# Optimization experiments

Hardware: AMD Instinct MI355X
Metric: run time of the kernel (lower is better)

Reference implementation:

```python
import jax, jax.numpy as jnp
import numpy as np

EPS = 1e-5


def conv2d(x, w, b, groups=1):
    # x: NCHW, w: OIHW, stride 1, SAME padding (== padding=k//2 for odd k)
    y = jax.lax.conv_general_dilated(
        x, w, window_strides=(1, 1), padding='SAME',
        dimension_numbers=('NCHW', 'OIHW', 'NCHW'),
        feature_group_count=groups)
    return y + b[None, :, None, None]


def gelu(x):
    return jax.nn.gelu(x, approximate=False)  # torch default GELU is exact erf


def adaptive_feature_norm(x, gamma, beta, s1w, s1b, s2w, s2b):
    # stats_net: GAP -> 1x1 conv -> ReLU -> 1x1 conv -> chunk into (gamma_a, beta_a)
    pooled = x.mean(axis=(2, 3), keepdims=True)                 # [B,C,1,1]
    h = jax.nn.relu(conv2d(pooled, s1w, s1b))
    stats = conv2d(h, s2w, s2b)                                 # [B,2C,1,1]
    ag, ab = jnp.split(stats, 2, axis=1)
    mean = x.mean(axis=(2, 3), keepdims=True)
    n = x.shape[2] * x.shape[3]
    var = ((x - mean) ** 2).sum(axis=(2, 3), keepdims=True) / (n - 1)  # unbiased, torch.var_mean default
    x_norm = (x - mean) * jax.lax.rsqrt(var + EPS)
    return (1 + ag) * gamma * x_norm + ab * beta


def setup_inputs() -> dict:
    key = jax.random.key(0)
    ks = jax.random.split(key, 40)
    B, C, H, W = 16, 256, 96, 96
    c4 = C // 4

    def n(k, shape, s=0.02):
        return jax.random.normal(k, shape, dtype=jnp.float32) * s

    inp = dict(
        x=jax.random.normal(ks[0], (B, C, H, W), dtype=jnp.float32),
        # branch1 conv1: dim -> dim//4, 3x3
        b1_conv1_w=n(ks[1], (c4, C, 3, 3)), b1_conv1_b=jnp.zeros((c4,), jnp.float32),
        # AFN on dim//4
        afn1_gamma=jnp.ones((1, c4, 1, 1), jnp.float32), afn1_beta=jnp.zeros((1, c4, 1, 1), jnp.float32),
        afn1_s1_w=n(ks[2], (c4 // 4, c4, 1, 1)), afn1_s1_b=jnp.zeros((c4 // 4,), jnp.float32),
        afn1_s2_w=n(ks[3], (c4 * 2, c4 // 4, 1, 1)), afn1_s2_b=jnp.zeros((c4 * 2,), jnp.float32),
        # branch1 conv2: dim//4 -> dim, 3x3
        b1_conv2_w=n(ks[4], (C, c4, 3, 3)), b1_conv2_b=jnp.zeros((C,), jnp.float32),
        # AFN on dim
        afn2_gamma=jnp.ones((1, C, 1, 1), jnp.float32), afn2_beta=jnp.zeros((1, C, 1, 1), jnp.float32),
        afn2_s1_w=n(ks[5], (c4, C, 1, 1)), afn2_s1_b=jnp.zeros((c4,), jnp.float32),
        afn2_s2_w=n(ks[6], (C * 2, c4, 1, 1)), afn2_s2_b=jnp.zeros((C * 2,), jnp.float32),
        # attention qkv/proj (1x1 convs)
        qkv_w=n(ks[7], (3 * C, C, 1, 1)), qkv_b=jnp.zeros((3 * C,), jnp.float32),
        proj_w=n(ks[8], (C, C, 1, 1)), proj_b=jnp.zeros((C,), jnp.float32),
        # 3 frequency decomposition branches, stacked
        # grouped 3x3 conv: groups=C//4, in=C (4 per group), out=C//4 (1 per group) -> weight [C//4, 4, 3, 3]
        fd_dw_w=n(ks[9], (3, c4, 4, 3, 3)), fd_dw_b=jnp.zeros((3, c4), jnp.float32),
        fd_pw_w=n(ks[10], (3, C, c4, 1, 1)), fd_pw_b=jnp.zeros((3, C), jnp.float32),
        freq_weights=jnp.ones((3,), jnp.float32),
        # router: GAP -> 1x1 conv -> softmax over 2 routes
        router_w=n(ks[11], (2, C, 1, 1)), router_b=jnp.zeros((2,), jnp.float32),
    )
    return inp


def reference(x,
              b1_conv1_w, b1_conv1_b, afn1_gamma, afn1_beta, afn1_s1_w, afn1_s1_b, afn1_s2_w, afn1_s2_b,
              b1_conv2_w, b1_conv2_b, afn2_gamma, afn2_beta, afn2_s1_w, afn2_s1_b, afn2_s2_w, afn2_s2_b,
              qkv_w, qkv_b, proj_w, proj_b, fd_dw_w, fd_dw_b, fd_pw_w, fd_pw_b, freq_weights,
              router_w, router_b):
    B, C, H, W = x.shape
    num_heads = 8
    hd = C // num_heads
    scale = C ** (-0.5)

    # ---- router ----
    pooled = x.mean(axis=(2, 3), keepdims=True)
    route = jax.nn.softmax(conv2d(pooled, router_w, router_b), axis=1)  # [B,2,1,1]

    # ---- branch1: conv -> AFN -> GELU -> conv -> AFN ----
    h = conv2d(x, b1_conv1_w, b1_conv1_b)
    h = adaptive_feature_norm(h, afn1_gamma, afn1_beta, afn1_s1_w, afn1_s1_b, afn1_s2_w, afn1_s2_b)
    h = gelu(h)
    h = conv2d(h, b1_conv2_w, b1_conv2_b)
    out1 = adaptive_feature_norm(h, afn2_gamma, afn2_beta, afn2_s1_w, afn2_s1_b, afn2_s2_w, afn2_s2_b)

    # ---- branch2: multi-scale frequency attention ----
    qkv = conv2d(x, qkv_w, qkv_b).reshape(B, 3, num_heads, hd, H, W)
    q, k, v = qkv[:, 0], qkv[:, 1], qkv[:, 2]          # [B, nh, hd, H, W]
    # attn over spatial rows: q @ k^T contracts W -> [B, nh, hd, H, H]
    attn = jnp.einsum('bndhw,bndgw->bndhg', q, k) * scale
    attn = jax.nn.softmax(attn, axis=-1)
    a = jnp.einsum('bndhg,bndgw->bndhw', attn, v)       # [B, nh, hd, H, W]
    # torch: .transpose(1, 2).reshape(B, C, H, W)  (hd-major channel order)
    a = a.transpose(0, 2, 1, 3, 4).reshape(B, C, H, W)
    x_attn = conv2d(a, proj_w, proj_b)

    fw = jax.nn.softmax(freq_weights, axis=0)
    freq_out = 0.0
    for i in range(3):
        f = conv2d(x, fd_dw_w[i], fd_dw_b[i], groups=C // 4)
        f = conv2d(gelu(f), fd_pw_w[i], fd_pw_b[i])
        freq_out = freq_out + fw[i] * f
    out2 = x_attn + freq_out

    return x + route[:, 0:1, :, :] * out1 + route[:, 1:2, :, :] * out2
```

## Files before the change

### kernel.cpp

```cpp
#include <hip/hip_runtime.h>
#include <hip/hip_bf16.h>
#include <math.h>
#include <stdint.h>

#define BB 16
#define CC 256
#define C4 64
#define HH 96
#define WW 96
#define HW 9216
#define EPSF 1e-5f

using bf16x8 = __attribute__((ext_vector_type(8))) short;
using bf16x4 = __attribute__((ext_vector_type(4))) short;
using f32x4  = __attribute__((ext_vector_type(4))) float;

#define GLD16(g, l) \
    __builtin_amdgcn_global_load_lds((const __attribute__((address_space(1))) unsigned int*)(g), \
                                     (__attribute__((address_space(3))) unsigned int*)(l), 16, 0, 0)

__device__ inline float bf2f_bits(short s) {
    return __uint_as_float(((unsigned int)(unsigned short)s) << 16);
}
__device__ inline short f2bf_bits(float f) {
    unsigned int u = __float_as_uint(f);
    return (short)((u + 0x7fffu + ((u >> 16) & 1u)) >> 16);
}

__global__ void zero_n_kernel(unsigned int* __restrict__ p, int n) {
    int i = blockIdx.x * 256 + threadIdx.x;
    if (i < n) p[i] = 0u;
}

__global__ void router_kernel(const float* __restrict__ pooled, const float* __restrict__ rw,
                              const float* __restrict__ rb, const float* __restrict__ fwts,
                              float* __restrict__ route, float* __restrict__ fw) {
    int t = threadIdx.x;
    const float invhw = 1.f / (float)HW;
    if (t < BB) {
        float l0 = rb[0], l1 = rb[1];
        for (int c = 0; c < CC; ++c) {
            float p = pooled[t * CC + c] * invhw;
            l0 += p * rw[c];
            l1 += p * rw[CC + c];
        }
        float m = fmaxf(l0, l1);
        float e0 = __expf(l0 - m), e1 = __expf(l1 - m);
        float inv = 1.f / (e0 + e1);
        route[t * 2 + 0] = e0 * inv;
        route[t * 2 + 1] = e1 * inv;
    }
    if (t == BB) {
        float a = fwts[0], b = fwts[1], c = fwts[2];
        float m = fmaxf(a, fmaxf(b, c));
        float e0 = __expf(a - m), e1 = __expf(b - m), e2 = __expf(c - m);
        float inv = 1.f / (e0 + e1 + e2);
        fw[0] = e0 * inv; fw[1] = e1 * inv; fw[2] = e2 * inv;
    }
}

__global__ void pack_w3x3_kernel(const float* __restrict__ w, __hip_bfloat16* __restrict__ wt,
                                 int COUT, int CINW) {
    int idx = blockIdx.x * 256 + threadIdx.x;
    int total = COUT * 9 * CINW;
    if (idx >= total) return;
    int ci = idx % CINW; int rest = idx / CINW; int tau = rest % 9; int co = rest / 9;
    wt[idx] = __float2bfloat16(w[((size_t)co * CINW + ci) * 9 + tau]);
}

__global__ void cast_w_kernel(const float* __restrict__ w, __hip_bfloat16* __restrict__ o, int n) {
    int idx = blockIdx.x * 256 + threadIdx.x;
    if (idx < n) o[idx] = __float2bfloat16(w[idx]);
}

__global__ void cast_w448_kernel(const float* __restrict__ w, __hip_bfloat16* __restrict__ A448) {
    int idx = blockIdx.x * 256 + threadIdx.x;
    int co = idx >> 8, ci = idx & 255;
    A448[co * 448 + ci] = __float2bfloat16(w[idx]);
}

__global__ void fuse_freq_w448_kernel(const float* __restrict__ pww, const float* __restrict__ pwb,
                                      const float* __restrict__ pjb, const float* __restrict__ fw,
                                      __hip_bfloat16* __restrict__ A448, float* __restrict__ fb448) {
    int co = blockIdx.x; int t = threadIdx.x;
    int i = t >> 6, g = t & 63;
    A448[co * 448 + 256 + t] = __float2bfloat16(fw[i] * pww[((size_t)(i * 256 + co)) * 64 + g]);
    if (t == 0) fb448[co] = pjb[co] + fw[0] * pwb[co] + fw[1] * pwb[256 + co] + fw[2] * pwb[512 + co];
}

__device__ inline float to_f32(float v) { return v; }
__device__ inline float to_f32(__hip_bfloat16 v) { return __bfloat162float(v); }

template <typename TIN, int CIN, int OSTR, bool POOL, bool AFN, bool GELU>
__global__ __launch_bounds__(256) void transpose_pm_kernel(const TIN* __restrict__ x,
                                                           __hip_bfloat16* __restrict__ xt,
                                                           float* __restrict__ pooled,
                                                           const float* __restrict__ mean,
                                                           const float* __restrict__ istd,
                                                           const float* __restrict__ ag,
                                                           const float* __restrict__ ab,
                                                           const float* __restrict__ gamma,
                                                           const float* __restrict__ beta) {
    __shared__ float s[32][33];
    __shared__ float ps[8][32];
    int p0 = blockIdx.x * 32, c0 = blockIdx.y * 32, b = blockIdx.z;
    int tx = threadIdx.x, ty = threadIdx.y;
    const TIN* xp = x + ((size_t)b * CIN + c0) * HW + p0;
#pragma unroll
    for (int i = 0; i < 4; ++i) {
        int c = ty * 4 + i;
        float v = to_f32(xp[(size_t)c * HW + tx]);
        if (AFN) {
            int bc = b * CIN + c0 + c;
            float sc = (1.f + ag[bc]) * gamma[c0 + c] * istd[bc];
            float sh = ab[bc] * beta[c0 + c];
            v = (v - mean[bc]) * sc + sh;
            if (GELU) v = 0.5f * v * (1.f + erff(v * 0.70710678118654752f));
        }
        s[c][tx] = v;
    }
    __syncthreads();
    __hip_bfloat16* yp = xt + ((size_t)b * HW + p0) * OSTR + c0;
#pragma unroll
    for (int i = 0; i < 4; ++i) {
        int r = ty * 4 + i;
        yp[(size_t)r * OSTR + tx] = __float2bfloat16(s[tx][r]);
    }
    if (POOL) {
        float l4 = 0.f;
#pragma unroll
        for (int i = 0; i < 4; ++i) l4 += s[tx][ty * 4 + i];
        ps[ty][tx] = l4;
        __syncthreads();
        if (ty == 0) {
            float tot = 0.f;
#pragma unroll
            for (int k = 0; k < 8; ++k) tot += ps[k][tx];
            atomicAdd(&pooled[b * CIN + c0 + tx], tot);
        }
    }
}

template <int KC, int CDIM, int CO_TOT>
__global__ __launch_bounds__(256) void conv3x3_kernel(const short* __restrict__ A,
                                                      const short* __restrict__ Bx,
                                                      const short* __restrict__ zp,
                                                      const float* __restrict__ bias,
                                                      float* __restrict__ Y,
                                                      float* __restrict__ ssum,
                                                      float* __restrict__ sssq) {
    constexpr int BM = 64, BN = 128, WN = 64;
    constexpr int FM = 2, FN = 4;
    constexpr int KBC = KC / 64;
    constexpr int NS = 3 * KBC;
    constexpr int SROWS = 160;
    __shared__ __align__(16) short Bs[2][SROWS * 64];
    int tid = threadIdx.x;
    int wid = tid >> 6, lane = tid & 63;
    int wy = wid >> 1, wx = wid & 1;
    int lane16 = lane & 15, quad = lane >> 4;
    int co0 = blockIdx.x * BM;
    int n0 = blockIdx.y * BN;
    int b = blockIdx.z;
    const short* Bbase = Bx + (size_t)b * HW * CDIM;

    bool m0[FN], m2[FN];
#pragma unroll
    for (int j = 0; j < FN; ++j) {
        int n = n0 + wx * WN + j * 16 + lane16;
        int w = n % 96;
        m0[j] = (w == 0);
        m2[j] = (w == 95);
    }

    int srow_l = lane >> 3;
    int schunk = (lane & 7) ^ srow_l;

    auto stage = [&](int s, int d) {
        int dh = s / KBC, kb = s - dh * KBC;
        int kc0 = kb * 64;
        int mb = n0 - 16 + (dh - 1) * 96;
#pragma unroll
        for (int t = 0; t < 5; ++t) {
            int inst = wid * 5 + t;
            int m = mb + inst * 8 + srow_l;
            const short* g = ((unsigned)m < (unsigned)HW)
                                 ? (Bbase + (size_t)m * CDIM + kc0 + schunk * 8)
                                 : zp;
            GLD16(g, &Bs[d][inst * 512]);
        }
    };

    f32x4 acc[FM][FN];
#pragma unroll
    for (int i = 0; i < FM; ++i)
#pragma unroll
        for (int j = 0; j < FN; ++j) acc[i][j] = (f32x4){0.f, 0.f, 0.f, 0.f};

    const bf16x8 Z8 = (bf16x8){0, 0, 0, 0, 0, 0, 0, 0};

    stage(0, 0);
    __syncthreads();
    for (int s = 0; s < NS; ++s) {
        int cur = s & 1;
        if (s + 1 < NS) stage(s + 1, cur ^ 1);
        int dh = s / KBC, kb = s - dh * KBC;
        int kc0 = kb * 64;
#pragma unroll
        for (int dw = 0; dw < 3; ++dw) {
            int tau = dh * 3 + dw;
            bf16x8 af[2][FM];
#pragma unroll
            for (int kk = 0; kk < 2; ++kk)
#pragma unroll
                for (int i = 0; i < FM; ++i)
                    af[kk][i] = *(const bf16x8*)(A + (size_t)(co0 + wy * 32 + i * 16 + lane16) * (9 * KC)
                                                 + tau * KC + kc0 + kk * 32 + quad * 8);
            bf16x8 bfr[2][FN];
#pragma unroll
            for (int kk = 0; kk < 2; ++kk)
#pragma unroll
                for (int j = 0; j < FN; ++j) {
                    int srow = wx * WN + j * 16 + lane16 + 15 + dw;
                    int cs = (quad + 4 * kk) ^ (srow & 7);
                    bf16x8 v = *(const bf16x8*)&Bs[cur][srow * 64 + cs * 8];
                    if (dw == 0) { if (m0[j]) v = Z8; }
                    else if (dw == 2) { if (m2[j]) v = Z8; }
                    bfr[kk][j] = v;
                }
#pragma unroll
            for (int kk = 0; kk < 2; ++kk)
#pragma unroll
                for (int i = 0; i < FM; ++i)
#pragma unroll
                    for (int j = 0; j < FN; ++j)
                        acc[i][j] = __builtin_amdgcn_mfma_f32_16x16x32_bf16(af[kk][i], bfr[kk][j],
                                                                            acc[i][j], 0, 0, 0);
        }
        __syncthreads();
    }

    float sl[FM][4], ql[FM][4];
#pragma unroll
    for (int i = 0; i < FM; ++i)
#pragma unroll
        for (int r = 0; r < 4; ++r) { sl[i][r] = 0.f; ql[i][r] = 0.f; }
#pragma unroll
    for (int i = 0; i < FM; ++i) {
        int co_l = co0 + wy * 32 + i * 16 + quad * 4;
#pragma unroll
        for (int j = 0; j < FN; ++j) {
            int pix = n0 + wx * WN + j * 16 + lane16;
#pragma unroll
            for (int r = 0; r < 4; ++r) {
                int co = co_l + r;
                float v = acc[i][j][r] + bias[co];
                Y[((size_t)(b * CO_TOT + co)) * HW + pix] = v;
                sl[i][r] += v; ql[i][r] += v * v;
            }
        }
    }
#pragma unroll
    for (int i = 0; i < FM; ++i) {
        int co_l = co0 + wy * 32 + i * 16 + quad * 4;
#pragma unroll
        for (int r = 0; r < 4; ++r) {
            float s = sl[i][r], q = ql[i][r];
            s += __shfl_xor(s, 1); q += __shfl_xor(q, 1);
            s += __shfl_xor(s, 2); q += __shfl_xor(q, 2);
            s += __shfl_xor(s, 4); q += __shfl_xor(q, 4);
            s += __shfl_xor(s, 8); q += __shfl_xor(q, 8);
            if (lane16 == 0) {
                int bc = b * CO_TOT + co_l + r;
                atomicAdd(&ssum[bc], s);
                atomicAdd(&sssq[bc], q);
            }
        }
    }
}

template <int BM, int BN, int KC, int CDIM, int EPI, int CO_TOT>
__global__ __launch_bounds__(256) void mfma_gemm_kernel(const short* __restrict__ A,
                                                        const short* __restrict__ Bx,
                                                        const short* __restrict__ zp,
                                                        const float* __restrict__ bias,
                                                        const float* __restrict__ route,
                                                        void* __restrict__ Y,
                                                        int bin0, int bout0) {
    constexpr int WM = BM / 2, WN = BN / 2;
    constexpr int FM = WM / 16, FN = WN / 16;
    constexpr int NS = KC / 64;
    constexpr int NA = BM / 16;
    constexpr int NB = BN / 16;
    __shared__ __align__(16) short As[2][2][BM * 32];
    __shared__ __align__(16) short Bs[2][2][BN * 32];
    int tid = threadIdx.x;
    int wid = tid >> 6, lane = tid & 63;
    int wy = wid >> 1, wx = wid & 1;
    int lane16 = lane & 15, quad = lane >> 4;
    int lrow = lane >> 2, lchk = lane & 3;
    int swz = (lrow >> 1) & 3;
    int co0 = blockIdx.x * BM;
    int n0 = blockIdx.y * BN;
    int bin = blockIdx.z + bin0;
    int bout = blockIdx.z + bout0;

    f32x4 acc[FM][FN];
#pragma unroll
    for (int i = 0; i < FM; ++i)
#pragma unroll
        for (int j = 0; j < FN; ++j) acc[i][j] = (f32x4){0.f, 0.f, 0.f, 0.f};

    const short* Bbase = Bx + (size_t)bin * HW * CDIM;

    auto stage = [&](int s, int d) {
        int kc0 = s * 64;
        int ksw = kc0 + (lchk ^ swz) * 8;
#pragma unroll
        for (int kk = 0; kk < 2; ++kk) {
#pragma unroll
            for (int t = 0; t < NA / 4; ++t) {
                int inst = wid * (NA / 4) + t;
                int row = inst * 16 + lrow;
                const short* g = A + (size_t)(co0 + row) * KC + ksw + kk * 32;
                GLD16(g, &As[d][kk][inst * 512]);
            }
#pragma unroll
            for (int t = 0; t < NB / 4; ++t) {
                int inst = wid * (NB / 4) + t;
                int row = inst * 16 + lrow;
                const short* g = Bbase + (size_t)(n0 + row) * CDIM + ksw + kk * 32;
                GLD16(g, &Bs[d][kk][inst * 512]);
            }
        }
    };

    stage(0, 0);
    __syncthreads();
    for (int s = 0; s < NS; ++s) {
        int cur = s & 1;
        if (s + 1 < NS) stage(s + 1, cur ^ 1);
#pragma unroll
        for (int kk = 0; kk < 2; ++kk) {
            bf16x8 af[FM], bfr[FN];
#pragma unroll
            for (int i = 0; i < FM; ++i) {
                int row = wy * WM + i * 16 + lane16;
                int ch = (quad ^ ((row >> 1) & 3)) * 8;
                af[i] = *(const bf16x8*)&As[cur][kk][row * 32 + ch];
            }
#pragma unroll
            for (int j = 0; j < FN; ++j) {
                int row = wx * WN + j * 16 + lane16;
                int ch = (quad ^ ((row >> 1) & 3)) * 8;
                bfr[j] = *(const bf16x8*)&Bs[cur][kk][row * 32 + ch];
            }
#pragma unroll
            for (int i = 0; i < FM; ++i)
#pragma unroll
                for (int j = 0; j < FN; ++j)
                    acc[i][j] = __builtin_amdgcn_mfma_f32_16x16x32_bf16(af[i], bfr[j], acc[i][j], 0, 0, 0);
        }
        __syncthreads();
    }

    float scale = 1.f;
    if (EPI == 2) scale = route[bin * 2 + 1];
#pragma unroll
    for (int i = 0; i < FM; ++i) {
        int co_l = co0 + wy * WM + i * 16 + quad * 4;
#pragma unroll
        for (int j = 0; j < FN; ++j) {
            int pix = n0 + wx * WN + j * 16 + lane16;
#pragma unroll
            for (int r = 0; r < 4; ++r) {
                int co = co_l + r;
                float v = acc[i][j][r] + bias[co];
                size_t idx = ((size_t)(bout * CO_TOT + co)) * HW + pix;
                if (EPI == 1) ((__hip_bfloat16*)Y)[idx] = __float2bfloat16(v);
                else ((float*)Y)[idx] += scale * v;
            }
        }
    }
}

__global__ void afn_finalize_kernel(const float* __restrict__ s, const float* __restrict__ q,
                                    float* __restrict__ mean, float* __restrict__ istd, int n) {
    int i = blockIdx.x * 256 + threadIdx.x;
    if (i >= n) return;
    float m = s[i] / (float)HW;
    float var = (q[i] - s[i] * m) / (float)(HW - 1);
    mean[i] = m;
    istd[i] = rsqrtf(var + EPSF);
}

template <int CH, int HID>
__global__ void afn_mlp_kernel(const float* __restrict__ mean,
                               const float* __restrict__ s1w, const float* __restrict__ s1b,
                               const float* __restrict__ s2w, const float* __restrict__ s2b,
                               float* __restrict__ ag, float* __restrict__ ab) {
    int b = blockIdx.x;
    __shared__ float hbuf[HID];
    int t = threadIdx.x;
    if (t < HID) {
        float s = s1b[t];
        for (int c = 0; c < CH; ++c) s += mean[b * CH + c] * s1w[t * CH + c];
        hbuf[t] = fmaxf(s, 0.f);
    }
    __syncthreads();
    if (t < 2 * CH) {
        float s = s2b[t];
#pragma unroll
        for (int k = 0; k < HID; ++k) s += hbuf[k] * s2w[t * HID + k];
        if (t < CH) ag[b * CH + t] = s;
        else        ab[b * CH + (t - CH)] = s;
    }
}

__global__ __launch_bounds__(256) void afn_combine_kernel(const float* __restrict__ x,
                                                          const float* __restrict__ h2,
                                                          const float* __restrict__ mean,
                                                          const float* __restrict__ istd,
                                                          const float* __restrict__ ag,
                                                          const float* __restrict__ ab,
                                                          const float* __restrict__ gamma,
                                                          const float* __restrict__ beta,
                                                          const float* __restrict__ route,
                                                          float* __restrict__ out) {
    int p4 = blockIdx.x * 256 + threadIdx.x;
    int c = blockIdx.y, b = blockIdx.z;
    int bc = b * CC + c;
    float scale = (1.f + ag[bc]) * gamma[c] * istd[bc];
    float shift = ab[bc] * beta[c];
    float m = mean[bc];
    float r0 = route[b * 2];
    size_t base = (size_t)bc * (HW / 4) + p4;
    const f32x4 xv = ((const f32x4*)x)[base];
    const f32x4 hv = ((const f32x4*)h2)[base];
    f32x4 o;
#pragma unroll
    for (int e = 0; e < 4; ++e) o[e] = xv[e] + r0 * ((hv[e] - m) * scale + shift);
    ((f32x4*)out)[base] = o;
}

__global__ __launch_bounds__(256) void vtrans_kernel(const __hip_bfloat16* __restrict__ qkv,
                                                     __hip_bfloat16* __restrict__ vt) {
    __shared__ __hip_bfloat16 s[32][34];
    int th = blockIdx.x / 3, tw = blockIdx.x % 3;
    int c = blockIdx.y, b = blockIdx.z;
    int tx = threadIdx.x, ty = threadIdx.y;
    const __hip_bfloat16* ip = qkv + ((size_t)b * 768 + 512 + c) * HW + (size_t)(th * 32) * 96 + tw * 32;
#pragma unroll
    for (int i = 0; i < 4; ++i) s[ty * 4 + i][tx] = ip[(size_t)(ty * 4 + i) * 96 + tx];
    __syncthreads();
    __hip_bfloat16* op = vt + ((size_t)b * 256 + c) * HW + (size_t)(tw * 32) * 96 + th * 32;
#pragma unroll
    for (int i = 0; i < 4; ++i) op[(size_t)(ty * 4 + i) * 96 + tx] = s[tx][ty * 4 + i];
}

__global__ __launch_bounds__(256) void attn_mfma_kernel(const __hip_bfloat16* __restrict__ qkv,
                                                        const __hip_bfloat16* __restrict__ vt,
                                                        __hip_bfloat16* __restrict__ a, int bout0) {
    int d = blockIdx.x, n = blockIdx.y, b = blockIdx.z;
    __shared__ __align__(16) __hip_bfloat16 Ps[96 * 104];
    int t = threadIdx.x;
    int lane = t & 63, wid = t >> 6;
    int wy = wid >> 1, wx = wid & 1;
    int lane16 = lane & 15, quad = lane >> 4;

    const __hip_bfloat16* qp = qkv + ((size_t)b * 768 + n * 32 + d) * HW;
    const __hip_bfloat16* kp = qp + (size_t)256 * HW;
    const __hip_bfloat16* vp = vt + ((size_t)b * 256 + n * 32 + d) * HW;

    f32x4 acc[3][3];
#pragma unroll
    for (int i = 0; i < 3; ++i)
#pragma unroll
        for (int j = 0; j < 3; ++j) acc[i][j] = (f32x4){0.f, 0.f, 0.f, 0.f};

#pragma unroll
    for (int kb = 0; kb < 3; ++kb) {
        int kc = kb * 32 + quad * 8;
        bf16x8 af[3], bfr[3];
#pragma unroll
        for (int i = 0; i < 3; ++i)
            af[i] = *(const bf16x8*)(qp + (size_t)(wy * 48 + i * 16 + lane16) * 96 + kc);
#pragma unroll
        for (int j = 0; j < 3; ++j)
            bfr[j] = *(const bf16x8*)(kp + (size_t)(wx * 48 + j * 16 + lane16) * 96 + kc);
#pragma unroll
        for (int i = 0; i < 3; ++i)
#pragma unroll
            for (int j = 0; j < 3; ++j)
                acc[i][j] = __builtin_amdgcn_mfma_f32_16x16x32_bf16(af[i], bfr[j], acc[i][j], 0, 0, 0);
    }

    const float scale = 0.0625f;
#pragma unroll
    for (int i = 0; i < 3; ++i) {
        int rbase = wy * 48 + i * 16 + quad * 4;
#pragma unroll
        for (int j = 0; j < 3; ++j) {
            int col = wx * 48 + j * 16 + lane16;
#pragma unroll
            for (int r = 0; r < 4; ++r)
                Ps[(rbase + r) * 104 + col] = __float2bfloat16(acc[i][j][r] * scale);
        }
    }
    __syncthreads();

    if (t < 192) {
        int row = t >> 1, hh = t & 1;
        const bf16x4* pr4 = (const bf16x4*)&Ps[row * 104 + hh * 48];
        float vb[48];
        float m = -1e30f;
#pragma unroll
        for (int j4 = 0; j4 < 12; ++j4) {
            bf16x4 u = pr4[j4];
#pragma unroll
            for (int e = 0; e < 4; ++e) {
                float f = bf2f_bits(u[e]);
                vb[j4 * 4 + e] = f;
                m = fmaxf(m, f);
            }
        }
        m = fmaxf(m, __shfl_xor(m, 1));
        float ssum = 0.f;
#pragma unroll
        for (int j2 = 0; j2 < 48; ++j2) { vb[j2] = __expf(vb[j2] - m); ssum += vb[j2]; }
        ssum += __shfl_xor(ssum, 1);
        float inv = 1.f / ssum;
        bf16x4* pw4 = (bf16x4*)&Ps[row * 104 + hh * 48];
#pragma unroll
        for (int j4 = 0; j4 < 12; ++j4) {
            bf16x4 o;
#pragma unroll
            for (int e = 0; e < 4; ++e) o[e] = f2bf_bits(vb[j4 * 4 + e] * inv);
            pw4[j4] = o;
        }
    }
    __syncthreads();

#pragma unroll
    for (int i = 0; i < 3; ++i)
#pragma unroll
        for (int j = 0; j < 3; ++j) acc[i][j] = (f32x4){0.f, 0.f, 0.f, 0.f};

#pragma unroll
    for (int kb = 0; kb < 3; ++kb) {
        int kc = kb * 32 + quad * 8;
        bf16x8 af[3], bfr[3];
#pragma unroll
        for (int i = 0; i < 3; ++i)
            af[i] = *(const bf16x8*)&Ps[(wy * 48 + i * 16 + lane16) * 104 + kc];
#pragma unroll
        for (int j = 0; j < 3; ++j)
            bfr[j] = *(const bf16x8*)(vp + (size_t)(wx * 48 + j * 16 + lane16) * 96 + kc);
#pragma unroll
        for (int i = 0; i < 3; ++i)
#pragma unroll
            for (int j = 0; j < 3; ++j)
                acc[i][j] = __builtin_amdgcn_mfma_f32_16x16x32_bf16(af[i], bfr[j], acc[i][j], 0, 0, 0);
    }

    __hip_bfloat16* ap = a + ((size_t)(bout0 + b) * CC + (d * 8 + n)) * HW;
#pragma unroll
    for (int i = 0; i < 3; ++i) {
        int rbase = wy * 48 + i * 16 + quad * 4;
#pragma unroll
        for (int j = 0; j < 3; ++j) {
            int col = wx * 48 + j * 16 + lane16;
#pragma unroll
            for (int r = 0; r < 4; ++r)
                ap[(size_t)(rbase + r) * 96 + col] = __float2bfloat16(acc[i][j][r]);
        }
    }
}

__global__ __launch_bounds__(256) void freq3_kernel(const float* __restrict__ x,
                                                    const float* __restrict__ dww,
                                                    const float* __restrict__ dwb,
                                                    __hip_bfloat16* __restrict__ f) {
    int p = blockIdx.x * 256 + threadIdx.x;
    int g = blockIdx.y;
    int b = blockIdx.z;
    int h = p / WW, w = p % WW;
    float a0 = dwb[g], a1 = dwb[64 + g], a2 = dwb[128 + g];
    const float* w0 = dww + g * 36;
    const float* w1 = dww + (64 + g) * 36;
    const float* w2 = dww + (128 + g) * 36;
#pragma unroll
    for (int q = 0; q < 4; ++q) {
        const float* xc = x + ((size_t)b * CC + 4 * g + q) * HW;
#pragma unroll
        for (int dh = 0; dh < 3; ++dh) {
            int hh = h + dh - 1;
            bool hv = (hh >= 0) && (hh < HH);
#pragma unroll
            for (int dw = 0; dw < 3; ++dw) {
                int ww2 = w + dw - 1;
                bool v = hv && (ww2 >= 0) && (ww2 < WW);
                float xv = v ? xc[hh * WW + ww2] : 0.f;
                int wi = q * 9 + dh * 3 + dw;
                a0 += xv * w0[wi];
                a1 += xv * w1[wi];
                a2 += xv * w2[wi];
            }
        }
    }
    a0 = 0.5f * a0 * (1.f + erff(a0 * 0.70710678118654752f));
    a1 = 0.5f * a1 * (1.f + erff(a1 * 0.70710678118654752f));
    a2 = 0.5f * a2 * (1.f + erff(a2 * 0.70710678118654752f));
    size_t base = ((size_t)b * 192 + g) * HW + p;
    f[base] = __float2bfloat16(a0);
    f[base + (size_t)64 * HW] = __float2bfloat16(a1);
    f[base + (size_t)128 * HW] = __float2bfloat16(a2);
}

extern "C" void kernel_launch(void* const* d_in, const int* in_sizes, int n_in,
                              void* d_out, int out_size, void* d_ws, size_t ws_size,
                              hipStream_t stream) {
    const float* x    = (const float*)d_in[0];
    const float* c1w  = (const float*)d_in[1];
    const float* c1b  = (const float*)d_in[2];
    const float* g1   = (const float*)d_in[3];
    const float* be1  = (const float*)d_in[4];
    const float* s1w1 = (const float*)d_in[5];
    const float* s1b1 = (const float*)d_in[6];
    const float* s2w1 = (const float*)d_in[7];
    const float* s2b1 = (const float*)d_in[8];
    const float* c2w  = (const float*)d_in[9];
    const float* c2b  = (const float*)d_in[10];
    const float* g2   = (const float*)d_in[11];
    const float* be2  = (const float*)d_in[12];
    const float* s1w2 = (const float*)d_in[13];
    const float* s1b2 = (const float*)d_in[14];
    const float* s2w2 = (const float*)d_in[15];
    const float* s2b2 = (const float*)d_in[16];
    const float* qkvw = (const float*)d_in[17];
    const float* qkvb = (const float*)d_in[18];
    const float* pjw  = (const float*)d_in[19];
    const float* pjb  = (const float*)d_in[20];
    const float* dww  = (const float*)d_in[21];
    const float* dwb  = (const float*)d_in[22];
    const float* pww  = (const float*)d_in[23];
    const float* pwb  = (const float*)d_in[24];
    const float* fwts = (const float*)d_in[25];
    const float* rw   = (const float*)d_in[26];
    const float* rb   = (const float*)d_in[27];
    float* out = (float*)d_out;
    (void)ws_size;

    char* ws = (char*)d_ws;
    float* h2 = (float*)ws;
    __hip_bfloat16* qkvs = (__hip_bfloat16*)ws;
    __hip_bfloat16* fall = (__hip_bfloat16*)ws;
    __hip_bfloat16* ftA = (__hip_bfloat16*)(ws + 56623104ULL);
    __hip_bfloat16* vt = (__hip_bfloat16*)(ws + 113246208ULL);
    float* h1 = (float*)(ws + 150994944ULL);
    __hip_bfloat16* h1t = (__hip_bfloat16*)(ws + 188743680ULL);
    __hip_bfloat16* xt = (__hip_bfloat16*)(ws + 207618048ULL);
    __hip_bfloat16* at = xt;
    const size_t TB = 283115520ULL;
    short* zp = (short*)(ws + TB);
    float* zf = (float*)(ws + TB + 256);
    float* ssum1  = zf;
    float* sssq1  = zf + 1024;
    float* ssum2  = zf + 2048;
    float* sssq2  = zf + 6144;
    float* pooled = zf + 10240;
    float* route  = zf + 14336;
    float* fw     = zf + 14368;
    float* mean1  = zf + 14372;
    float* istd1  = zf + 15396;
    float* ag1    = zf + 16420;
    float* ab1    = zf + 17444;
    float* mean2  = zf + 18468;
    float* istd2  = zf + 22564;
    float* ag2    = zf + 26660;
    float* ab2    = zf + 30756;
    float* fb448  = zf + 34852;
    char* wbase = (char*)(zf + 35108);
    __hip_bfloat16* wt1  = (__hip_bfloat16*)wbase;
    __hip_bfloat16* wt2  = (__hip_bfloat16*)(wbase + 294912);
    __hip_bfloat16* qw16 = (__hip_bfloat16*)(wbase + 589824);
    __hip_bfloat16* A448 = (__hip_bfloat16*)(wbase + 983040);

    zero_n_kernel<<<57, 256, 0, stream>>>((unsigned int*)zp, 14400);

    transpose_pm_kernel<float, 256, 256, true, false, false>
        <<<dim3(288, 8, 16), dim3(32, 8), 0, stream>>>(x, xt, pooled, nullptr, nullptr,
                                                       nullptr, nullptr, nullptr, nullptr);
    router_kernel<<<1, 64, 0, stream>>>(pooled, rw, rb, fwts, route, fw);

    pack_w3x3_kernel<<<576, 256, 0, stream>>>(c1w, wt1, 64, 256);
    pack_w3x3_kernel<<<576, 256, 0, stream>>>(c2w, wt2, 256, 64);
    cast_w_kernel<<<768, 256, 0, stream>>>(qkvw, qw16, 768 * 256);
    cast_w448_kernel<<<256, 256, 0, stream>>>(pjw, A448);
    fuse_freq_w448_kernel<<<256, 192, 0, stream>>>(pww, pwb, pjb, fw, A448, fb448);

    conv3x3_kernel<256, 256, 64>
        <<<dim3(1, 72, 16), 256, 0, stream>>>((const short*)wt1, (const short*)xt, zp, c1b,
                                              h1, ssum1, sssq1);
    afn_finalize_kernel<<<4, 256, 0, stream>>>(ssum1, sssq1, mean1, istd1, BB * C4);
    afn_mlp_kernel<64, 16><<<dim3(BB), 128, 0, stream>>>(mean1, s1w1, s1b1, s2w1, s2b1, ag1, ab1);
    transpose_pm_kernel<float, 64, 64, false, true, true>
        <<<dim3(288, 2, 16), dim3(32, 8), 0, stream>>>(h1, h1t, nullptr, mean1, istd1,
                                                       ag1, ab1, g1, be1);
    conv3x3_kernel<64, 64, 256>
        <<<dim3(4, 72, 16), 256, 0, stream>>>((const short*)wt2, (const short*)h1t, zp, c2b,
                                              h2, ssum2, sssq2);
    afn_finalize_kernel<<<16, 256, 0, stream>>>(ssum2, sssq2, mean2, istd2, BB * CC);
    afn_mlp_kernel<256, 64><<<dim3(BB), 512, 0, stream>>>(mean2, s1w2, s1b2, s2w2, s2b2, ag2, ab2);
    afn_combine_kernel<<<dim3(9, 256, 16), 256, 0, stream>>>(x, h2, mean2, istd2, ag2, ab2,
                                                             g2, be2, route, out);

    for (int half = 0; half < 2; ++half) {
        mfma_gemm_kernel<128, 128, 256, 256, 1, 768>
            <<<dim3(6, 72, 8), 256, 0, stream>>>((const short*)qw16, (const short*)xt, zp, qkvb,
                                                 nullptr, qkvs, half * 8, 0);
        vtrans_kernel<<<dim3(9, 256, 8), dim3(32, 8), 0, stream>>>(qkvs, vt);
        attn_mfma_kernel<<<dim3(32, 8, 8), 256, 0, stream>>>(qkvs, vt, at, half * 8);
    }

    freq3_kernel<<<dim3(36, 64, 16), 256, 0, stream>>>(x, dww, dwb, fall);

    transpose_pm_kernel<__hip_bfloat16, 256, 448, false, false, false>
        <<<dim3(288, 8, 16), dim3(32, 8), 0, stream>>>(at, ftA, nullptr, nullptr, nullptr,
                                                       nullptr, nullptr, nullptr, nullptr);
    transpose_pm_kernel<__hip_bfloat16, 192, 448, false, false, false>
        <<<dim3(288, 6, 16), dim3(32, 8), 0, stream>>>(fall, ftA + 256, nullptr, nullptr, nullptr,
                                                       nullptr, nullptr, nullptr, nullptr);

    mfma_gemm_kernel<128, 128, 448, 448, 2, 256>
        <<<dim3(2, 72, 16), 256, 0, stream>>>((const short*)A448, (const short*)ftA, zp, fb448,
                                              route, out, 0, 0);
}
```

Baseline: 1.239 ms.

## Prefetch conv A fragments into registers, add K=64 single-stage conv kernel

The general 3x3 conv kernel now prefetches the next stage's weight fragments into a double-buffered register array. It replaces __syncthreads with explicit vmcnt waits plus raw barriers, so global loads overlap the MFMA work. A new specialised kernel for the 64-input-channel conv loads the whole halo tile and all 9 taps of weights up front, then runs every tap without further syncs. The 1x1 GEMM uses the same partial vmcnt wait scheme. This raises register pressure (36 weight fragments held in registers), and the hand-written vmcnt counts must match the number of loads issued per stage.

```diff
diff --git a/kernel.cpp b/kernel.cpp
--- a/kernel.cpp
+++ b/kernel.cpp
@@ -18,6 +18,13 @@
 #define GLD16(g, l) \
     __builtin_amdgcn_global_load_lds((const __attribute__((address_space(1))) unsigned int*)(g), \
                                      (__attribute__((address_space(3))) unsigned int*)(l), 16, 0, 0)
+
+template <int N> __device__ inline void wait_vm() {
+    if constexpr (N == 0) asm volatile("s_waitcnt vmcnt(0)" ::: "memory");
+    else if constexpr (N == 5) asm volatile("s_waitcnt vmcnt(5)" ::: "memory");
+    else if constexpr (N == 8) asm volatile("s_waitcnt vmcnt(8)" ::: "memory");
+    else static_assert(N == 0 || N == 5 || N == 8, "unsupported vmcnt");
+}
 
 __device__ inline float bf2f_bits(short s) {
     return __uint_as_float(((unsigned int)(unsigned short)s) << 16);
@@ -191,31 +198,31 @@
         }
     };
 
-    f32x4 acc[FM][FN];
-#pragma unroll
-    for (int i = 0; i < FM; ++i)
-#pragma unroll
-        for (int j = 0; j < FN; ++j) acc[i][j] = (f32x4){0.f, 0.f, 0.f, 0.f};
-
-    const bf16x8 Z8 = (bf16x8){0, 0, 0, 0, 0, 0, 0, 0};
-
-    stage(0, 0);
-    __syncthreads();
-    for (int s = 0; s < NS; ++s) {
-        int cur = s & 1;
-        if (s + 1 < NS) stage(s + 1, cur ^ 1);
+    auto loadA = [&](bf16x8 (&ar)[12], int s) {
         int dh = s / KBC, kb = s - dh * KBC;
         int kc0 = kb * 64;
+        const short* Ab = A + (size_t)(co0 + wy * 32 + lane16) * (9 * KC) + dh * 3 * KC + kc0 + quad * 8;
+#pragma unroll
+        for (int dw = 0; dw < 3; ++dw)
+#pragma unroll
+            for (int kk = 0; kk < 2; ++kk)
+#pragma unroll
+                for (int i = 0; i < FM; ++i)
+                    ar[dw * 4 + kk * 2 + i] =
+                        *(const bf16x8*)(Ab + dw * KC + kk * 32 + (size_t)i * 16 * (9 * KC));
+    };
+
+    f32x4 acc[FM][FN];
+#pragma unroll
+    for (int i = 0; i < FM; ++i)
+#pragma unroll
+        for (int j = 0; j < FN; ++j) acc[i][j] = (f32x4){0.f, 0.f, 0.f, 0.f};
+
+    const bf16x8 Z8 = (bf16x8){0, 0, 0, 0, 0, 0, 0, 0};
+
+    auto compute = [&](bf16x8 (&ar)[12], int cur) {
 #pragma unroll
         for (int dw = 0; dw < 3; ++dw) {
-            int tau = dh * 3 + dw;
-            bf16x8 af[2][FM];
-#pragma unroll
-            for (int kk = 0; kk < 2; ++kk)
-#pragma unroll
-                for (int i = 0; i < FM; ++i)
-                    af[kk][i] = *(const bf16x8*)(A + (size_t)(co0 + wy * 32 + i * 16 + lane16) * (9 * KC)
-                                                 + tau * KC + kc0 + kk * 32 + quad * 8);
             bf16x8 bfr[2][FN];
 #pragma unroll
             for (int kk = 0; kk < 2; ++kk)
@@ -234,11 +241,159 @@
                 for (int i = 0; i < FM; ++i)
 #pragma unroll
                     for (int j = 0; j < FN; ++j)
-                        acc[i][j] = __builtin_amdgcn_mfma_f32_16x16x32_bf16(af[kk][i], bfr[kk][j],
-                                                                            acc[i][j], 0, 0, 0);
-        }
-        __syncthreads();
-    }
+                        acc[i][j] = __builtin_amdgcn_mfma_f32_16x16x32_bf16(ar[dw * 4 + kk * 2 + i],
+                                                                            bfr[kk][j], acc[i][j], 0, 0, 0);
+        }
+    };
+
+    bf16x8 arA[12], arB[12];
+    loadA(arA, 0);
+    stage(0, 0);
+    for (int s = 0; s < NS; ++s) {
+        int cur = s & 1;
+        if (s + 1 < NS) { stage(s + 1, cur ^ 1); wait_vm<5>(); }
+        else            { wait_vm<0>(); }
+        __builtin_amdgcn_s_barrier();
+        __builtin_amdgcn_sched_barrier(0);
+        if (s + 1 < NS) loadA(cur ? arA : arB, s + 1);
+        if (cur == 0) compute(arA, 0); else compute(arB, 1);
+        __builtin_amdgcn_sched_barrier(0);
+        __builtin_amdgcn_s_barrier();
+    }
+
+    float sl[FM][4], ql[FM][4];
+#pragma unroll
+    for (int i = 0; i < FM; ++i)
+#pragma unroll
+        for (int r = 0; r < 4; ++r) { sl[i][r] = 0.f; ql[i][r] = 0.f; }
+#pragma unroll
+    for (int i = 0; i < FM; ++i) {
+        int co_l = co0 + wy * 32 + i * 16 + quad * 4;
+#pragma unroll
+        for (int j = 0; j < FN; ++j) {
+            int pix = n0 + wx * WN + j * 16 + lane16;
+#pragma unroll
+            for (int r = 0; r < 4; ++r) {
+                int co = co_l + r;
+                float v = acc[i][j][r] + bias[co];
+                Y[((size_t)(b * CO_TOT + co)) * HW + pix] = v;
+                sl[i][r] += v; ql[i][r] += v * v;
+            }
+        }
+    }
+#pragma unroll
+    for (int i = 0; i < FM; ++i) {
+        int co_l = co0 + wy * 32 + i * 16 + quad * 4;
+#pragma unroll
+        for (int r = 0; r < 4; ++r) {
+            float s = sl[i][r], q = ql[i][r];
+            s += __shfl_xor(s, 1); q += __shfl_xor(q, 1);
+            s += __shfl_xor(s, 2); q += __shfl_xor(q, 2);
+            s += __shfl_xor(s, 4); q += __shfl_xor(q, 4);
+            s += __shfl_xor(s, 8); q += __shfl_xor(q, 8);
+            if (lane16 == 0) {
+                int bc = b * CO_TOT + co_l + r;
+                atomicAdd(&ssum[bc], s);
+                atomicAdd(&sssq[bc], q);
+            }
+        }
+    }
+}
+
+template <int CO_TOT>
+__global__ __launch_bounds__(256) void conv3x3_k64_kernel(const short* __restrict__ A,
+                                                          const short* __restrict__ Bx,
+                                                          const short* __restrict__ zp,
+                                                          const float* __restrict__ bias,
+                                                          float* __restrict__ Y,
+                                                          float* __restrict__ ssum,
+                                                          float* __restrict__ sssq) {
+    constexpr int BM = 64, BN = 128, WN = 64;
+    constexpr int FM = 2, FN = 4;
+    constexpr int SROWS = 352;
+    __shared__ __align__(16) short Bs[SROWS * 64];
+    int tid = threadIdx.x;
+    int wid = tid >> 6, lane = tid & 63;
+    int wy = wid >> 1, wx = wid & 1;
+    int lane16 = lane & 15, quad = lane >> 4;
+    int co0 = blockIdx.x * BM;
+    int n0 = blockIdx.y * BN;
+    int b = blockIdx.z;
+    const short* Bbase = Bx + (size_t)b * HW * 64;
+
+    bool m0[FN], m2[FN];
+#pragma unroll
+    for (int j = 0; j < FN; ++j) {
+        int n = n0 + wx * WN + j * 16 + lane16;
+        int w = n % 96;
+        m0[j] = (w == 0);
+        m2[j] = (w == 95);
+    }
+
+    int srow_l = lane >> 3;
+    int schunk = (lane & 7) ^ srow_l;
+
+#pragma unroll
+    for (int t = 0; t < 11; ++t) {
+        int inst = wid * 11 + t;
+        int m = n0 - 112 + inst * 8 + srow_l;
+        const short* g = ((unsigned)m < (unsigned)HW)
+                             ? (Bbase + (size_t)m * 64 + schunk * 8)
+                             : zp;
+        GLD16(g, &Bs[inst * 512]);
+    }
+
+    bf16x8 ar[36];
+    {
+        const short* Ab = A + (size_t)(co0 + wy * 32 + lane16) * (9 * 64) + quad * 8;
+#pragma unroll
+        for (int tau = 0; tau < 9; ++tau)
+#pragma unroll
+            for (int kk = 0; kk < 2; ++kk)
+#pragma unroll
+                for (int i = 0; i < FM; ++i)
+                    ar[tau * 4 + kk * 2 + i] =
+                        *(const bf16x8*)(Ab + tau * 64 + kk * 32 + (size_t)i * 16 * (9 * 64));
+    }
+
+    f32x4 acc[FM][FN];
+#pragma unroll
+    for (int i = 0; i < FM; ++i)
+#pragma unroll
+        for (int j = 0; j < FN; ++j) acc[i][j] = (f32x4){0.f, 0.f, 0.f, 0.f};
+
+    const bf16x8 Z8 = (bf16x8){0, 0, 0, 0, 0, 0, 0, 0};
+
+    wait_vm<0>();
+    __builtin_amdgcn_s_barrier();
+    __builtin_amdgcn_sched_barrier(0);
+
+#pragma unroll
+    for (int dh = 0; dh < 3; ++dh)
+#pragma unroll
+        for (int dw = 0; dw < 3; ++dw) {
+            int tau = dh * 3 + dw;
+            bf16x8 bfr[2][FN];
+#pragma unroll
+            for (int kk = 0; kk < 2; ++kk)
+#pragma unroll
+                for (int j = 0; j < FN; ++j) {
+                    int srow = wx * WN + j * 16 + lane16 + dh * 96 + dw + 15;
+                    int cs = (quad + 4 * kk) ^ (srow & 7);
+                    bf16x8 v = *(const bf16x8*)&Bs[srow * 64 + cs * 8];
+                    if (dw == 0) { if (m0[j]) v = Z8; }
+                    else if (dw == 2) { if (m2[j]) v = Z8; }
+                    bfr[kk][j] = v;
+                }
+#pragma unroll
+            for (int kk = 0; kk < 2; ++kk)
+#pragma unroll
+                for (int i = 0; i < FM; ++i)
+#pragma unroll
+                    for (int j = 0; j < FN; ++j)
+                        acc[i][j] = __builtin_amdgcn_mfma_f32_16x16x32_bf16(ar[tau * 4 + kk * 2 + i],
+                                                                            bfr[kk][j], acc[i][j], 0, 0, 0);
+        }
 
     float sl[FM][4], ql[FM][4];
 #pragma unroll
@@ -336,10 +491,12 @@
     };
 
     stage(0, 0);
-    __syncthreads();
     for (int s = 0; s < NS; ++s) {
         int cur = s & 1;
-        if (s + 1 < NS) stage(s + 1, cur ^ 1);
+        if (s + 1 < NS) { stage(s + 1, cur ^ 1); wait_vm<8>(); }
+        else            { wait_vm<0>(); }
+        __builtin_amdgcn_s_barrier();
+        __builtin_amdgcn_sched_barrier(0);
 #pragma unroll
         for (int kk = 0; kk < 2; ++kk) {
             bf16x8 af[FM], bfr[FN];
@@ -361,7 +518,8 @@
                 for (int j = 0; j < FN; ++j)
                     acc[i][j] = __builtin_amdgcn_mfma_f32_16x16x32_bf16(af[i], bfr[j], acc[i][j], 0, 0, 0);
         }
-        __syncthreads();
+        __builtin_amdgcn_sched_barrier(0);
+        __builtin_amdgcn_s_barrier();
     }
 
     float scale = 1.f;
@@ -707,7 +865,7 @@
     transpose_pm_kernel<float, 64, 64, false, true, true>
         <<<dim3(288, 2, 16), dim3(32, 8), 0, stream>>>(h1, h1t, nullptr, mean1, istd1,
                                                        ag1, ab1, g1, be1);
-    conv3x3_kernel<64, 64, 256>
+    conv3x3_k64_kernel<256>
         <<<dim3(4, 72, 16), 256, 0, stream>>>((const short*)wt2, (const short*)h1t, zp, c2b,
                                               h2, ssum2, sssq2);
     afn_finalize_kernel<<<16, 256, 0, stream>>>(ssum2, sssq2, mean2, istd2, BB * CC);
```

Result: slower. 1.343 ms (+8.4%).
